# Optimization experiments

Measured on AMD Instinct MI355X. Metric: run time of the kernel, lower is better.

## Reference

```python
import jax, jax.numpy as jnp
import numpy as np

DIM = 256
HALF = DIM // 2
B, S = 32, 4096
U_MAX = 4096          # upper bound on number of unique tree positions (positions < S)
MAX_DEPTH = 13        # bitlen(S) covers all path lengths for positions <= S


def setup_inputs() -> dict:
    key = jax.random.key(0)
    k1, k2, k3, k4, k5 = jax.random.split(key, 5)
    token_types = jax.random.randint(k1, (B, S), 0, 5, dtype=jnp.int32)
    node_positions = jax.random.randint(k2, (B, S), 0, S, dtype=jnp.int32)
    small_vals = jax.random.randint(k3, (B, S), 0, 4, dtype=jnp.int32)
    # deBruijn tokens (type 4) reference tree positions -> values must lie in unique(node_positions)
    token_values = jnp.where(token_types == 4, node_positions,
                   jnp.where(token_types == 3, -1, small_vals)).astype(jnp.int32)
    primitives = jax.random.normal(k4, (2, HALF, HALF), dtype=jnp.float32)
    identity = jnp.ones((1, HALF), dtype=jnp.float32)
    embed_weight = jax.random.normal(k5, (11, HALF), dtype=jnp.float32)
    return {"token_types": token_types, "token_values": token_values,
            "node_positions": node_positions, "primitives": primitives,
            "identity": identity, "embed_weight": embed_weight}


def cayley(X):
    # torch orthogonal(..., orthogonal_map='cayley'): A = tril(X) - tril(X)^T (skew), Q = (I - A/2)^{-1}(I + A/2)
    A = jnp.tril(X)
    A = A - jnp.swapaxes(A, -1, -2)
    I = jnp.eye(X.shape[-1], dtype=X.dtype)
    return jnp.linalg.solve(I - 0.5 * A, I + 0.5 * A)


def _forward(token_types, token_values, node_positions, primitives, identity, embed_weight):
    Q = cayley(primitives)                                   # [2, h, h] orthogonal maps
    flat_pos = node_positions.ravel()
    uniq, inv = jnp.unique(flat_pos, return_inverse=True, size=U_MAX, fill_value=S)
    inv = inv.ravel()

    # binary path of pos: bit d of pos for d < bitlen(pos)-1, padded with 2 (pos<=1 -> empty path)
    d = jnp.arange(MAX_DEPTH, dtype=uniq.dtype)
    bits = (uniq[:, None] >> d) & 1                           # [U, D]
    valid = (uniq[:, None] >> (d + 1)) > 0
    word = jnp.where(valid, bits, 2)                          # [U, D]

    maps0 = jnp.broadcast_to(identity, (U_MAX, HALF)).astype(primitives.dtype)

    def step(maps, b):                                        # maps [U, h], b [U]
        m0 = maps @ Q[0].T                                    # linear(maps, primitives[0])
        m1 = maps @ Q[1].T
        maps = jnp.where((b == 0)[:, None], m0,
                jnp.where((b == 1)[:, None], m1, maps))
        return maps, None

    path_emb, _ = jax.lax.scan(step, maps0, word.T)           # [U, h]

    pos_enc = path_emb[inv].reshape(B, S, HALF)               # positional encodings

    sos = token_types == 0
    bop = token_types == 1
    nop = token_types == 2
    oos = (token_types == 3) & (token_values == -1)
    db = token_types == 4

    emb_idx = jnp.where(bop, token_values + 1,
              jnp.where(nop, token_values + 5, 0))
    type_emb = embed_weight[emb_idx]                          # [B, S, h]

    db_idx = jnp.searchsorted(uniq, jnp.clip(token_values, 0, S - 1))  # bucketize into unique positions
    db_emb = path_emb[db_idx]                                 # [B, S, h]

    content = jnp.zeros_like(pos_enc)
    content = jnp.where(sos[..., None], embed_weight[0], content)
    content = jnp.where((bop | nop)[..., None], type_emb, content)
    content = jnp.where(db[..., None], db_emb, content)
    content = jnp.where(oos[..., None], embed_weight[10], content)

    return jnp.concatenate([content, pos_enc], axis=-1)       # [B, S, DIM]


def reference(token_types, token_values, node_positions, primitives, identity, embed_weight):
    return _forward(token_types, token_values, node_positions, primitives, identity, embed_weight)
```

## Files before the change

### kernel.cpp

```cpp
#include <hip/hip_runtime.h>

#define HALF 128
#define NMAT 16384
#define NTOK 131072

__global__ __launch_bounds__(512) void cayley_qt(const float* __restrict__ prim,
                                                 float* __restrict__ QT) {
    __shared__ __align__(16) float Xs[128 * 129];
    __shared__ __align__(16) float CpT[2][16][132];
    __shared__ __align__(16) float Rp [2][16][128];
    __shared__ __align__(16) float Dcol[2][16][20];

    const int b = blockIdx.x;
    const float* __restrict__ X = prim + b * NMAT;
    const int t  = threadIdx.x;
    const int c  = t & 127;
    const int q  = t >> 7;
    const int r0 = q << 5;

    for (int idx4 = t; idx4 < 4096; idx4 += 512) {
        int gi = idx4 << 2;
        float4 v = *(const float4*)(X + gi);
        int r = gi >> 7, cc = gi & 127;
        float* p = &Xs[r * 129 + cc];
        p[0] = v.x; p[1] = v.y; p[2] = v.z; p[3] = v.w;
    }
    __syncthreads();

    float reg[32];
    #pragma unroll
    for (int i = 0; i < 32; ++i) {
        int r  = r0 + i;
        int mx = r > c ? r : c;
        int mn = r ^ c ^ mx;
        float x = Xs[mx * 129 + mn];
        reg[i] = (r == c) ? 1.0f : (r > c ? 0.5f * x : -0.5f * x);
    }

    #pragma unroll
    for (int s = 0; s < 8; ++s) {
        const int  p     = s & 1;
        const int  k0    = s << 4;
        const int  q0    = s >> 1;
        const int  kl    = (s & 1) << 4;
        const bool panel = (c >= k0) && (c < k0 + 16);

        if (panel) {
            const int m = c - k0;
            #pragma unroll
            for (int i = 0; i < 32; i += 4)
                *(float4*)&CpT[p][m][r0 + i] =
                    make_float4(reg[i], reg[i+1], reg[i+2], reg[i+3]);
        }
        if (q == q0) {
            #pragma unroll
            for (int j = 0; j < 16; ++j) Rp[p][j][c] = reg[kl + j];
        }
        __syncthreads();

        if (t < 64) {
            const int cp = t & 15, q4 = t >> 4;
            float dd[4];
            #pragma unroll
            for (int i = 0; i < 4; ++i) dd[i] = Rp[p][q4 * 4 + i][k0 + cp];
            #pragma unroll
            for (int k = 0; k < 16; ++k) {
                float cv[4];
                #pragma unroll
                for (int i = 0; i < 4; ++i) cv[i] = __shfl(dd[i], (q4 << 4) | k);
                float rv   = __shfl(dd[k & 3], ((k >> 2) << 4) | cp);
                float dkk  = __shfl(rv, k);
                float dinv = 1.0f / dkk;
                float sv   = rv * dinv;
                bool  own  = (cp == k);
                float rf   = own ? dinv : sv;
                #pragma unroll
                for (int i = 0; i < 4; ++i)
                    dd[i] = own ? (-dd[i] * dinv) : fmaf(-cv[i], sv, dd[i]);
                dd[k & 3] = (q4 == (k >> 2)) ? rf : dd[k & 3];
            }
            #pragma unroll
            for (int i = 0; i < 4; ++i) Dcol[p][cp][q4 * 4 + i] = dd[i];
        }
        __syncthreads();

        float coeff[16];
        if (!panel) {
            #pragma unroll
            for (int j = 0; j < 16; ++j) coeff[j] = 0.0f;
            #pragma unroll
            for (int j = 0; j < 16; ++j) {
                float rpj = Rp[p][j][c];
                #pragma unroll
                for (int mq = 0; mq < 16; mq += 4) {
                    float4 dv = *(const float4*)&Dcol[p][j][mq];
                    coeff[mq+0] = fmaf(dv.x, rpj, coeff[mq+0]);
                    coeff[mq+1] = fmaf(dv.y, rpj, coeff[mq+1]);
                    coeff[mq+2] = fmaf(dv.z, rpj, coeff[mq+2]);
                    coeff[mq+3] = fmaf(dv.w, rpj, coeff[mq+3]);
                }
            }
        } else {
            const int mp = c - k0;
            #pragma unroll
            for (int j = 0; j < 16; ++j) coeff[j] = Dcol[p][mp][j];
            #pragma unroll
            for (int i = 0; i < 32; ++i) reg[i] = 0.0f;
        }

        #pragma unroll
        for (int m = 0; m < 16; ++m) {
            float cm = coeff[m];
            #pragma unroll
            for (int i = 0; i < 32; i += 4) {
                float4 c4 = *(const float4*)&CpT[p][m][r0 + i];
                reg[i+0] = fmaf(-c4.x, cm, reg[i+0]);
                reg[i+1] = fmaf(-c4.y, cm, reg[i+1]);
                reg[i+2] = fmaf(-c4.z, cm, reg[i+2]);
                reg[i+3] = fmaf(-c4.w, cm, reg[i+3]);
            }
        }
        if (q == q0) {
            #pragma unroll
            for (int j = 0; j < 16; ++j) reg[kl + j] = coeff[j];
        }
    }

    float* __restrict__ out = QT + b * NMAT;
    #pragma unroll
    for (int i = 0; i < 32; ++i) {
        int r = r0 + i;
        out[r * HALF + c] = 2.0f * reg[i] - (r == c ? 1.0f : 0.0f);
    }
}

__global__ __launch_bounds__(256) void path_steps(const float* __restrict__ QT,
                                                  const float* __restrict__ ident,
                                                  float* __restrict__ P,
                                                  int vbase, int d0) {
    __shared__ float vs[2][8][HALF];
    const int t    = threadIdx.x;
    const int rg   = t >> 5;
    const int jj   = (t & 31) << 2;
    const int v    = vbase + (blockIdx.x << 3) + rg;
    const int vmax = vbase + (blockIdx.x << 3) + 7;

    float4 sv;
    if (d0 == 0) {
        sv = *(const float4*)&ident[jj];
    } else {
        const int u = (v & 127) | 128;
        sv = *(const float4*)&P[u * HALF + jj];
    }
    *(float4*)&vs[0][rg][jj] = sv;
    __syncthreads();

    int cur = 0;
    for (int d = d0; d < 13; ++d) {
        if ((vmax >> (d + 1)) == 0) break;
        const bool valid = (v >> (d + 1)) > 0;
        const float* __restrict__ Qm = QT + (((v >> d) & 1) ? NMAT : 0);
        float4 acc = make_float4(0.f, 0.f, 0.f, 0.f);
        #pragma unroll 4
        for (int cc = 0; cc < 128; cc += 4) {
            float4 v4 = *(const float4*)&vs[cur][rg][cc];
            float4 q0 = *(const float4*)&Qm[(cc+0)*HALF + jj];
            float4 q1 = *(const float4*)&Qm[(cc+1)*HALF + jj];
            float4 q2 = *(const float4*)&Qm[(cc+2)*HALF + jj];
            float4 q3 = *(const float4*)&Qm[(cc+3)*HALF + jj];
            acc.x = fmaf(v4.x,q0.x, fmaf(v4.y,q1.x, fmaf(v4.z,q2.x, fmaf(v4.w,q3.x, acc.x))));
            acc.y = fmaf(v4.x,q0.y, fmaf(v4.y,q1.y, fmaf(v4.z,q2.y, fmaf(v4.w,q3.y, acc.y))));
            acc.z = fmaf(v4.x,q0.z, fmaf(v4.y,q1.z, fmaf(v4.z,q2.z, fmaf(v4.w,q3.z, acc.z))));
            acc.w = fmaf(v4.x,q0.w, fmaf(v4.y,q1.w, fmaf(v4.z,q2.w, fmaf(v4.w,q3.w, acc.w))));
        }
        if (!valid) acc = *(const float4*)&vs[cur][rg][jj];
        *(float4*)&vs[cur ^ 1][rg][jj] = acc;
        __syncthreads();
        cur ^= 1;
    }
    *(float4*)&P[v * HALF + jj] = *(const float4*)&vs[cur][rg][jj];
}

__global__ __launch_bounds__(256) void emit_out(const int* __restrict__ tt,
                                                const int* __restrict__ tv,
                                                const int* __restrict__ np,
                                                const float* __restrict__ P,
                                                const float* __restrict__ emb,
                                                float* __restrict__ out) {
    const int i  = (blockIdx.x << 2) + (threadIdx.x >> 6);
    const int jj = (threadIdx.x & 63) << 2;
    const int ty = tt[i];
    const int v  = tv[i];
    float4 val;
    if (jj < 128) {
        if (ty == 0)      val = *(const float4*)&emb[jj];
        else if (ty == 1) val = *(const float4*)&emb[(v + 1) * HALF + jj];
        else if (ty == 2) val = *(const float4*)&emb[(v + 5) * HALF + jj];
        else if (ty == 4) {
            int vc = v < 0 ? 0 : (v > 4095 ? 4095 : v);
            val = *(const float4*)&P[vc * HALF + jj];
        } else val = (v == -1) ? *(const float4*)&emb[10 * HALF + jj]
                               : make_float4(0.f, 0.f, 0.f, 0.f);
    } else {
        const int p = np[i];
        val = *(const float4*)&P[p * HALF + (jj - 128)];
    }
    *(float4*)&out[i * 256 + jj] = val;
}

extern "C" void kernel_launch(void* const* d_in, const int* in_sizes, int n_in,
                              void* d_out, int out_size, void* d_ws, size_t ws_size,
                              hipStream_t stream) {
    const int*   token_types = (const int*)  d_in[0];
    const int*   token_vals  = (const int*)  d_in[1];
    const int*   node_pos    = (const int*)  d_in[2];
    const float* prim        = (const float*)d_in[3];
    const float* ident       = (const float*)d_in[4];
    const float* emb         = (const float*)d_in[5];
    float* out = (float*)d_out;

    float* QT = (float*)d_ws;
    float* P  = (float*)((char*)d_ws + 262144);

    cayley_qt  <<<2,   512, 0, stream>>>(prim, QT);
    path_steps <<<32,  256, 0, stream>>>(QT, ident, P, 0,   0);
    path_steps <<<480, 256, 0, stream>>>(QT, ident, P, 256, 7);
    emit_out   <<<NTOK / 4, 256, 0, stream>>>(token_types, token_vals, node_pos,
                                              P, emb, out);
}
```

Baseline: 296.5 us.

## Split path kernel, stage Q matrix in shared memory, use nontemporal output stores

Replaces the generic path_steps kernel with two specialised kernels. path_base handles positions below 256 with 64 blocks of four rows each, every thread computing two columns, which spreads the serial base work across more CUs. path_upper exploits the fact that all rows in a block share the same upper path bits, so it loads the 64KB Q matrix into shared memory once per depth step rather than streaming it from global or L2. emit_out now writes its output with nontemporal stores to avoid polluting the cache. The costs are large LDS use per block, which limits occupancy, and an extra full-matrix copy for every depth step.

```diff
diff --git a/kernel.cpp b/kernel.cpp
--- a/kernel.cpp
+++ b/kernel.cpp
@@ -3,6 +3,8 @@
 #define HALF 128
 #define NMAT 16384
 #define NTOK 131072
+
+typedef float f4 __attribute__((ext_vector_type(4)));
 
 __global__ __launch_bounds__(512) void cayley_qt(const float* __restrict__ prim,
                                                  float* __restrict__ QT) {
@@ -134,51 +136,82 @@
     }
 }
 
-__global__ __launch_bounds__(256) void path_steps(const float* __restrict__ QT,
-                                                  const float* __restrict__ ident,
-                                                  float* __restrict__ P,
-                                                  int vbase, int d0) {
-    __shared__ float vs[2][8][HALF];
+__global__ __launch_bounds__(256) void path_base(const float* __restrict__ QT,
+                                                 const float* __restrict__ ident,
+                                                 float* __restrict__ P) {
+    __shared__ __align__(16) float vs[2][4][HALF];
     const int t    = threadIdx.x;
-    const int rg   = t >> 5;
-    const int jj   = (t & 31) << 2;
-    const int v    = vbase + (blockIdx.x << 3) + rg;
-    const int vmax = vbase + (blockIdx.x << 3) + 7;
-
-    float4 sv;
-    if (d0 == 0) {
-        sv = *(const float4*)&ident[jj];
-    } else {
-        const int u = (v & 127) | 128;
-        sv = *(const float4*)&P[u * HALF + jj];
-    }
-    *(float4*)&vs[0][rg][jj] = sv;
+    const int rg   = t >> 6;
+    const int jj   = (t & 63) << 1;
+    const int v    = (blockIdx.x << 2) + rg;
+    const int vmax = (blockIdx.x << 2) + 3;
+
+    float2 cv = *(const float2*)&ident[jj];
+    *(float2*)&vs[0][rg][jj] = cv;
     __syncthreads();
 
     int cur = 0;
-    for (int d = d0; d < 13; ++d) {
+    for (int d = 0; d < 8; ++d) {
         if ((vmax >> (d + 1)) == 0) break;
         const bool valid = (v >> (d + 1)) > 0;
         const float* __restrict__ Qm = QT + (((v >> d) & 1) ? NMAT : 0);
+        float2 acc = make_float2(0.f, 0.f);
+        #pragma unroll 4
+        for (int cc = 0; cc < 128; cc += 4) {
+            float4 v4 = *(const float4*)&vs[cur][rg][cc];
+            float2 q0 = *(const float2*)&Qm[(cc+0)*HALF + jj];
+            float2 q1 = *(const float2*)&Qm[(cc+1)*HALF + jj];
+            float2 q2 = *(const float2*)&Qm[(cc+2)*HALF + jj];
+            float2 q3 = *(const float2*)&Qm[(cc+3)*HALF + jj];
+            acc.x = fmaf(v4.x,q0.x, fmaf(v4.y,q1.x, fmaf(v4.z,q2.x, fmaf(v4.w,q3.x, acc.x))));
+            acc.y = fmaf(v4.x,q0.y, fmaf(v4.y,q1.y, fmaf(v4.z,q2.y, fmaf(v4.w,q3.y, acc.y))));
+        }
+        if (valid) cv = acc;
+        *(float2*)&vs[cur ^ 1][rg][jj] = cv;
+        __syncthreads();
+        cur ^= 1;
+    }
+    *(float2*)&P[v * HALF + jj] = cv;
+}
+
+__global__ __launch_bounds__(256) void path_upper(const float* __restrict__ QT,
+                                                  float* __restrict__ P) {
+    __shared__ __align__(16) float Qs[128 * 128];
+    __shared__ __align__(16) float vs[8][HALF];
+    const int t  = threadIdx.x;
+    const int rg = t >> 5;
+    const int jj = (t & 31) << 2;
+    const int k  = 2 + (blockIdx.x >> 4);
+    const int r  = ((blockIdx.x & 15) << 3) + rg;
+    const int v  = (k << 7) | r;
+
+    float4 cv = *(const float4*)&P[(128 + r) * HALF + jj];
+
+    for (int d = 7; d < 13; ++d) {
+        if ((k >> (d - 6)) == 0) break;
+        const float* __restrict__ Qm = QT + (((k >> (d - 7)) & 1) ? NMAT : 0);
+        *(float4*)&vs[rg][jj] = cv;
+        __syncthreads();
+        for (int i = t; i < 4096; i += 256)
+            *(float4*)&Qs[i << 2] = *(const float4*)&Qm[i << 2];
+        __syncthreads();
+
         float4 acc = make_float4(0.f, 0.f, 0.f, 0.f);
         #pragma unroll 4
         for (int cc = 0; cc < 128; cc += 4) {
-            float4 v4 = *(const float4*)&vs[cur][rg][cc];
-            float4 q0 = *(const float4*)&Qm[(cc+0)*HALF + jj];
-            float4 q1 = *(const float4*)&Qm[(cc+1)*HALF + jj];
-            float4 q2 = *(const float4*)&Qm[(cc+2)*HALF + jj];
-            float4 q3 = *(const float4*)&Qm[(cc+3)*HALF + jj];
+            float4 v4 = *(const float4*)&vs[rg][cc];
+            float4 q0 = *(const float4*)&Qs[(cc+0)*HALF + jj];
+            float4 q1 = *(const float4*)&Qs[(cc+1)*HALF + jj];
+            float4 q2 = *(const float4*)&Qs[(cc+2)*HALF + jj];
+            float4 q3 = *(const float4*)&Qs[(cc+3)*HALF + jj];
             acc.x = fmaf(v4.x,q0.x, fmaf(v4.y,q1.x, fmaf(v4.z,q2.x, fmaf(v4.w,q3.x, acc.x))));
             acc.y = fmaf(v4.x,q0.y, fmaf(v4.y,q1.y, fmaf(v4.z,q2.y, fmaf(v4.w,q3.y, acc.y))));
             acc.z = fmaf(v4.x,q0.z, fmaf(v4.y,q1.z, fmaf(v4.z,q2.z, fmaf(v4.w,q3.z, acc.z))));
             acc.w = fmaf(v4.x,q0.w, fmaf(v4.y,q1.w, fmaf(v4.z,q2.w, fmaf(v4.w,q3.w, acc.w))));
         }
-        if (!valid) acc = *(const float4*)&vs[cur][rg][jj];
-        *(float4*)&vs[cur ^ 1][rg][jj] = acc;
-        __syncthreads();
-        cur ^= 1;
-    }
-    *(float4*)&P[v * HALF + jj] = *(const float4*)&vs[cur][rg][jj];
+        cv = acc;
+    }
+    *(float4*)&P[v * HALF + jj] = cv;
 }
 
 __global__ __launch_bounds__(256) void emit_out(const int* __restrict__ tt,
@@ -191,21 +224,21 @@
     const int jj = (threadIdx.x & 63) << 2;
     const int ty = tt[i];
     const int v  = tv[i];
-    float4 val;
+    f4 val;
     if (jj < 128) {
-        if (ty == 0)      val = *(const float4*)&emb[jj];
-        else if (ty == 1) val = *(const float4*)&emb[(v + 1) * HALF + jj];
-        else if (ty == 2) val = *(const float4*)&emb[(v + 5) * HALF + jj];
+        if (ty == 0)      val = *(const f4*)&emb[jj];
+        else if (ty == 1) val = *(const f4*)&emb[(v + 1) * HALF + jj];
+        else if (ty == 2) val = *(const f4*)&emb[(v + 5) * HALF + jj];
         else if (ty == 4) {
             int vc = v < 0 ? 0 : (v > 4095 ? 4095 : v);
-            val = *(const float4*)&P[vc * HALF + jj];
-        } else val = (v == -1) ? *(const float4*)&emb[10 * HALF + jj]
-                               : make_float4(0.f, 0.f, 0.f, 0.f);
+            val = *(const f4*)&P[vc * HALF + jj];
+        } else if (v == -1) val = *(const f4*)&emb[10 * HALF + jj];
+        else { f4 z = {0.f, 0.f, 0.f, 0.f}; val = z; }
     } else {
         const int p = np[i];
-        val = *(const float4*)&P[p * HALF + (jj - 128)];
-    }
-    *(float4*)&out[i * 256 + jj] = val;
+        val = *(const f4*)&P[p * HALF + (jj - 128)];
+    }
+    __builtin_nontemporal_store(val, (f4*)&out[i * 256 + jj]);
 }
 
 extern "C" void kernel_launch(void* const* d_in, const int* in_sizes, int n_in,
@@ -223,8 +256,8 @@
     float* P  = (float*)((char*)d_ws + 262144);
 
     cayley_qt  <<<2,   512, 0, stream>>>(prim, QT);
-    path_steps <<<32,  256, 0, stream>>>(QT, ident, P, 0,   0);
-    path_steps <<<480, 256, 0, stream>>>(QT, ident, P, 256, 7);
+    path_base  <<<64,  256, 0, stream>>>(QT, ident, P);
+    path_upper <<<480, 256, 0, stream>>>(QT, P);
     emit_out   <<<NTOK / 4, 256, 0, stream>>>(token_types, token_vals, node_pos,
                                               P, emb, out);
 }
```

Result: faster. 280.0 us (-5.6%).
